# Kernel tuning notes

Measured on AMD Instinct MI355X. Metric: run time of the kernel, lower is better.

The kernel has to match this reference:

```python
import jax, jax.numpy as jnp
import numpy as np
import math

D_MODEL = 512
NUM_HEADS = 8
D_HEAD = D_MODEL // NUM_HEADS
B, S = 4, 2048
L = 2 * S - 1  # relative position range


def _rel_shift(pos_score):
    # pos_score: [B, H, S, L] -> [B, H, S, L//2+1] via pad/reshape/slice trick
    b, h, s, l = pos_score.shape
    padded = jnp.pad(pos_score, ((0, 0), (0, 0), (0, 0), (1, 0)))  # [B,H,S,L+1]
    padded = padded.reshape(b, h, l + 1, s)
    shifted = padded[:, :, 1:].reshape(b, h, s, l)
    return shifted[..., : l // 2 + 1]


def setup_inputs() -> dict:
    key = jax.random.key(0)
    ks = jax.random.split(key, 16)
    std = 1.0 / math.sqrt(D_MODEL)
    inp = {
        "query": jax.random.normal(ks[0], (B, S, D_MODEL), jnp.float32),
        "key": jax.random.normal(ks[1], (B, S, D_MODEL), jnp.float32),
        "value": jax.random.normal(ks[2], (B, S, D_MODEL), jnp.float32),
        "pos_embedding": jax.random.normal(ks[3], (B, L, D_MODEL), jnp.float32),
        "Wq": jax.random.normal(ks[4], (D_MODEL, D_MODEL), jnp.float32) * std,
        "bq": jnp.zeros((D_MODEL,), jnp.float32),
        "Wk": jax.random.normal(ks[5], (D_MODEL, D_MODEL), jnp.float32) * std,
        "bk": jnp.zeros((D_MODEL,), jnp.float32),
        "Wv": jax.random.normal(ks[6], (D_MODEL, D_MODEL), jnp.float32) * std,
        "bv": jnp.zeros((D_MODEL,), jnp.float32),
        "Wp": jax.random.normal(ks[7], (D_MODEL, D_MODEL), jnp.float32) * std,
        "u_bias": jax.random.normal(ks[8], (NUM_HEADS, D_HEAD), jnp.float32) * std,
        "v_bias": jax.random.normal(ks[9], (NUM_HEADS, D_HEAD), jnp.float32) * std,
        "Wo": jax.random.normal(ks[10], (D_MODEL, D_MODEL), jnp.float32) * std,
        "bo": jnp.zeros((D_MODEL,), jnp.float32),
    }
    return inp


def reference(query, key, value, pos_embedding, Wq, bq, Wk, bk, Wv, bv, Wp, u_bias, v_bias, Wo, bo):
    b, s, d = query.shape
    h, dh = u_bias.shape
    sqrt_dim = jnp.asarray(math.sqrt(d), query.dtype)

    q = (query @ Wq.T + bq).reshape(b, s, h, dh)
    k = (key @ Wk.T + bk).reshape(b, -1, h, dh)
    v = (value @ Wv.T + bv).reshape(b, -1, h, dh)
    p = (pos_embedding @ Wp.T).reshape(b, -1, h, dh)

    content_score = jnp.einsum("bshd,bthd->bhst", q + u_bias, k)
    pos_score = jnp.einsum("bshd,blhd->bhsl", q + v_bias, p)
    pos_score = _rel_shift(pos_score)  # [B,H,S,S]

    score = (content_score + pos_score) / sqrt_dim
    attn = jax.nn.softmax(score, axis=-1)
    context = jnp.einsum("bhst,bthd->bshd", attn, v).reshape(b, s, d)
    return context @ Wo.T + bo
```

## Files before the change

### kernel.cpp

```cpp
#include <hip/hip_runtime.h>


typedef __bf16 bf16;
typedef __bf16 bf16x4 __attribute__((ext_vector_type(4)));
typedef __bf16 bf16x8 __attribute__((ext_vector_type(8)));
typedef float  f32x4  __attribute__((ext_vector_type(4)));

#define MFMA(A,B,C) __builtin_amdgcn_mfma_f32_16x16x32_bf16((A),(B),(C),0,0,0)

constexpr float SCP = 1.44269504088896f / 22.6274169979695f;

__device__ __forceinline__ void gload16(const void* g, void* l) {
    __builtin_amdgcn_global_load_lds(
        (const __attribute__((address_space(1))) void*)g,
        (__attribute__((address_space(3))) void*)l, 16, 0, 0);
}

constexpr size_t WBYTES   = 512u*512u*2u;
constexpr size_t OFF_WQ   = 0;
constexpr size_t OFF_WK   = OFF_WQ + WBYTES;
constexpr size_t OFF_WV   = OFF_WK + WBYTES;
constexpr size_t OFF_WP   = OFF_WV + WBYTES;
constexpr size_t OFF_WO   = OFF_WP + WBYTES;
constexpr size_t QKV_BYTES = 4ull*8*2048*64*2;
constexpr size_t OFF_QU   = OFF_WO + WBYTES;
constexpr size_t OFF_QV   = OFF_QU + QKV_BYTES;
constexpr size_t OFF_KK   = OFF_QV + QKV_BYTES;
constexpr size_t OFF_VT   = OFF_KK + QKV_BYTES;
constexpr size_t OFF_PP   = OFF_VT + QKV_BYTES;
constexpr size_t PP_BYTES = 4ull*8*4096*64*2;
constexpr size_t OFF_CTX  = OFF_PP + PP_BYTES;

__global__ __launch_bounds__(256) void convert_weights(
    const float* __restrict__ w0, const float* __restrict__ w1,
    const float* __restrict__ w2, const float* __restrict__ w3,
    const float* __restrict__ w4, bf16* __restrict__ dst)
{
    int idx = blockIdx.x * 256 + threadIdx.x;
    const float* srcs[5] = {w0, w1, w2, w3, w4};
    int which = idx >> 15;
    int off   = (idx & 32767) * 8;
    const float* s = srcs[which] + off;
    float4 a = *(const float4*)s;
    float4 b = *(const float4*)(s + 4);
    bf16x8 o;
    o[0]=(bf16)a.x; o[1]=(bf16)a.y; o[2]=(bf16)a.z; o[3]=(bf16)a.w;
    o[4]=(bf16)b.x; o[5]=(bf16)b.y; o[6]=(bf16)b.z; o[7]=(bf16)b.w;
    *(bf16x8*)(dst + (size_t)which * (512*512) + off) = o;
}

__global__ __launch_bounds__(256) void gemm_proj(
    const float* __restrict__ Aq, const float* __restrict__ Ak,
    const float* __restrict__ Av, const float* __restrict__ Ap,
    const bf16* __restrict__ Wqb, const bf16* __restrict__ Wkb,
    const bf16* __restrict__ Wvb, const bf16* __restrict__ Wpb,
    const float* __restrict__ bq, const float* __restrict__ bk,
    const float* __restrict__ bv,
    const float* __restrict__ ub, const float* __restrict__ vb,
    bf16* __restrict__ qu, bf16* __restrict__ qv, bf16* __restrict__ kk,
    bf16* __restrict__ vt, bf16* __restrict__ pp)
{
    const int bid = blockIdx.x;
    const int mode = (bid < 768) ? (bid >> 8) : 3;
    const int idx  = (bid < 768) ? (bid & 255) : (bid - 768);
    const float* A  = (mode == 0) ? Aq  : (mode == 1) ? Ak  : (mode == 2) ? Av  : Ap;
    const bf16*  Bw = (mode == 0) ? Wqb : (mode == 1) ? Wkb : (mode == 2) ? Wvb : Wpb;

    __shared__ __align__(16) bf16 As[128 * 64];
    const int tid = threadIdx.x, lane = tid & 63, w = tid >> 6;
    const int r = lane & 15, g = lane >> 4;
    const int m0 = (idx >> 2) * 128, n0 = (idx & 3) * 128;
    const int wr = (w >> 1) * 64, wc = (w & 1) * 64;
    f32x4 acc[4][4] = {};

    for (int kt = 0; kt < 512; kt += 64) {
        __syncthreads();
        #pragma unroll
        for (int i = 0; i < 4; i++) {
            int gi = tid + 256 * i;
            int row = gi >> 3, c8 = gi & 7;
            int gm = m0 + row;
            float4 a0 = {0,0,0,0}, a1 = {0,0,0,0};
            if (mode != 3 || gm < 16380) {
                const float* ap = A + (size_t)gm * 512 + kt + c8 * 8;
                a0 = *(const float4*)ap;
                a1 = *(const float4*)(ap + 4);
            }
            bf16x8 v8;
            v8[0]=(bf16)a0.x; v8[1]=(bf16)a0.y; v8[2]=(bf16)a0.z; v8[3]=(bf16)a0.w;
            v8[4]=(bf16)a1.x; v8[5]=(bf16)a1.y; v8[6]=(bf16)a1.z; v8[7]=(bf16)a1.w;
            *(bf16x8*)((char*)As + row * 128 + ((c8 ^ (row & 7)) << 4)) = v8;
        }
        __syncthreads();
        #pragma unroll
        for (int ks = 0; ks < 2; ks++) {
            bf16x8 af[4], bfr[4];
            #pragma unroll
            for (int rt = 0; rt < 4; rt++) {
                int row = wr + rt * 16 + r;
                af[rt] = *(const bf16x8*)((const char*)As + row * 128 +
                                          (((ks * 4 + g) ^ (row & 7)) << 4));
            }
            #pragma unroll
            for (int ct = 0; ct < 4; ct++) {
                int n = n0 + wc + ct * 16 + r;
                bfr[ct] = *(const bf16x8*)(Bw + (size_t)n * 512 + kt + ks * 32 + g * 8);
            }
            #pragma unroll
            for (int rt = 0; rt < 4; rt++)
                #pragma unroll
                for (int ct = 0; ct < 4; ct++)
                    acc[rt][ct] = MFMA(af[rt], bfr[ct], acc[rt][ct]);
        }
    }

    #pragma unroll
    for (int rt = 0; rt < 4; rt++) {
        #pragma unroll
        for (int ct = 0; ct < 4; ct++) {
            int gn = n0 + wc + ct * 16 + r;
            int rb = m0 + wr + rt * 16 + g * 4;
            #pragma unroll
            for (int i = 0; i < 4; i++) {
                int gm = rb + i;
                float val = acc[rt][ct][i];
                if (mode == 0) {
                    int b = gm >> 11, s = gm & 2047, h = gn >> 6, dh = gn & 63;
                    size_t o = ((size_t)((b * 8 + h) * 2048 + s)) * 64 + dh;
                    float qb = val + bq[gn];
                    qu[o] = (bf16)((qb + ub[gn]) * SCP);
                    qv[o] = (bf16)((qb + vb[gn]) * SCP);
                } else if (mode == 1) {
                    int b = gm >> 11, s = gm & 2047, h = gn >> 6, dh = gn & 63;
                    kk[((size_t)((b * 8 + h) * 2048 + s)) * 64 +
                       (dh ^ ((s & 7) << 3))] = (bf16)(val + bk[gn]);
                } else if (mode == 2) {
                    int b = gm >> 11, s = gm & 2047, h = gn >> 6, dh = gn & 63;
                    int sc = s & 63, sb = s & ~63;
                    vt[((size_t)((b * 8 + h) * 64 + dh)) * 2048 + sb +
                       (sc ^ ((dh & 7) << 3))] = (bf16)(val + bv[gn]);
                } else {
                    if (gm < 16380) {
                        int b = gm / 4095, l = gm - b * 4095, h = gn >> 6, dh = gn & 63;
                        pp[((size_t)((b * 8 + h) * 4096 + l)) * 64 + dh] = (bf16)val;
                    }
                }
            }
        }
    }
}

__global__ __launch_bounds__(256) void gemm_out(
    const bf16* __restrict__ Ac, const bf16* __restrict__ Bw,
    const float* __restrict__ bias, float* __restrict__ of)
{
    __shared__ __align__(16) bf16 As[128 * 64];
    const int tid = threadIdx.x, lane = tid & 63, w = tid >> 6;
    const int r = lane & 15, g = lane >> 4;
    const int m0 = blockIdx.x * 128, n0 = blockIdx.y * 128;
    const int wr = (w >> 1) * 64, wc = (w & 1) * 64;
    f32x4 acc[4][4] = {};

    for (int kt = 0; kt < 512; kt += 64) {
        __syncthreads();
        #pragma unroll
        for (int i = 0; i < 4; i++) {
            int gi = tid + 256 * i;
            int row = gi >> 3, c8 = gi & 7;
            bf16x8 v8 = *(const bf16x8*)(Ac + (size_t)(m0 + row) * 512 + kt + c8 * 8);
            *(bf16x8*)((char*)As + row * 128 + ((c8 ^ (row & 7)) << 4)) = v8;
        }
        __syncthreads();
        #pragma unroll
        for (int ks = 0; ks < 2; ks++) {
            bf16x8 af[4], bfr[4];
            #pragma unroll
            for (int rt = 0; rt < 4; rt++) {
                int row = wr + rt * 16 + r;
                af[rt] = *(const bf16x8*)((const char*)As + row * 128 +
                                          (((ks * 4 + g) ^ (row & 7)) << 4));
            }
            #pragma unroll
            for (int ct = 0; ct < 4; ct++) {
                int n = n0 + wc + ct * 16 + r;
                bfr[ct] = *(const bf16x8*)(Bw + (size_t)n * 512 + kt + ks * 32 + g * 8);
            }
            #pragma unroll
            for (int rt = 0; rt < 4; rt++)
                #pragma unroll
                for (int ct = 0; ct < 4; ct++)
                    acc[rt][ct] = MFMA(af[rt], bfr[ct], acc[rt][ct]);
        }
    }
    #pragma unroll
    for (int rt = 0; rt < 4; rt++)
        #pragma unroll
        for (int ct = 0; ct < 4; ct++) {
            int gn = n0 + wc + ct * 16 + r;
            int rb = m0 + wr + rt * 16 + g * 4;
            #pragma unroll
            for (int i = 0; i < 4; i++)
                of[(size_t)(rb + i) * 512 + gn] = acc[rt][ct][i] + bias[gn];
        }
}

__global__ __launch_bounds__(512, 2) void attn_k(
    const bf16* __restrict__ qu, const bf16* __restrict__ qv,
    const bf16* __restrict__ kk, const bf16* __restrict__ vt,
    const bf16* __restrict__ pp, bf16* __restrict__ ctx)
{
    __shared__ __align__(16) bf16 kls[2][64 * 64];
    __shared__ __align__(16) bf16 vls[3][64 * 64];
    __shared__ __align__(16) bf16 ps2[256][100];
    __shared__ __align__(16) bf16 at_t[256 * 64];

    const int lane = threadIdx.x & 63, w = threadIdx.x >> 6;
    const int r = lane & 15, g = lane >> 4;
    const int sw = (r & 7) << 4;
    const int bid = blockIdx.x;
    const int lbid = (bid & 7) * 32 + (bid >> 3);
    const int bh = lbid >> 3;
    const int sigma = lbid & 7;
    const int s0 = sigma << 8;
    const int qb = w << 5;

    const bf16* quB = qu + (size_t)bh * 2048 * 64;
    const bf16* qvB = qv + (size_t)bh * 2048 * 64;
    const bf16* kkB = kk + (size_t)bh * 2048 * 64;
    const bf16* vtB = vt + (size_t)bh * 64 * 2048;
    const bf16* ppB = pp + (size_t)bh * 4096 * 64;

    bf16x8 qaf[2][2], qvf[2][2];
    #pragma unroll
    for (int qs = 0; qs < 2; qs++) {
        const int srow = s0 + qb + qs * 16 + r;
        qaf[qs][0] = *(const bf16x8*)(quB + (size_t)srow * 64 + g * 8);
        qaf[qs][1] = *(const bf16x8*)(quB + (size_t)srow * 64 + 32 + g * 8);
        qvf[qs][0] = *(const bf16x8*)(qvB + (size_t)srow * 64 + g * 8);
        qvf[qs][1] = *(const bf16x8*)(qvB + (size_t)srow * 64 + 32 + g * 8);
    }
    __builtin_amdgcn_sched_barrier(0);

    const int lq = lane >> 3, lc = (lane & 7) << 4;

    bf16x8 pfP[12];
    {
        const int tp = ((sigma * 4) & 31) << 6;
        gload16((const char*)kkB + ((size_t)(tp + w * 8 + lq) << 7) + lc,
                (char*)kls[0] + w * 1024);
        gload16((const char*)vtB + ((size_t)(w * 8 + lq) << 12) + tp * 2 + lc,
                (char*)vls[0] + w * 1024);
        __builtin_amdgcn_sched_barrier(0);
        const int lbw = tp - s0 - qb + 2016;
        #pragma unroll
        for (int j = 0; j < 6; j++) {
            const bf16* pr = ppB + (size_t)(lbw + j * 16 + r) * 64 + g * 8;
            pfP[2*j]   = *(const bf16x8*)pr;
            pfP[2*j+1] = *(const bf16x8*)(pr + 32);
        }
        asm volatile("s_waitcnt vmcnt(0)" ::: "memory");
        __builtin_amdgcn_s_barrier();
        __builtin_amdgcn_sched_barrier(0);
    }

    f32x4 oacc[2][4] = {};
    float sums[2] = {0.f, 0.f};
    int iv_prev = 2, iv_cur = 0, iv_next = 1;

    #pragma unroll 2
    for (int n = 0; n < 32; ++n) {
        const int cur = n & 1;
        if (n > 0) {
            __builtin_amdgcn_s_barrier();
            __builtin_amdgcn_sched_barrier(0);
        }

        {
            const int tn = ((sigma * 4 + n + 1) & 31) << 6;
            gload16((const char*)kkB + ((size_t)(tn + w * 8 + lq) << 7) + lc,
                    (char*)kls[cur ^ 1] + w * 1024);
            gload16((const char*)vtB + ((size_t)(w * 8 + lq) << 12) + tn * 2 + lc,
                    (char*)vls[iv_next] + w * 1024);
        }
        __builtin_amdgcn_sched_barrier(0);

        if (n > 0) {
            const char* vbase = (const char*)vls[iv_prev];
            #pragma unroll
            for (int ks = 0; ks < 2; ks++) {
                bf16x8 af[2];
                #pragma unroll
                for (int qs = 0; qs < 2; qs++)
                    af[qs] = *(const bf16x8*)((const char*)at_t +
                               (qb + qs * 16 + r) * 128 + ((ks * 64 + g * 16) ^ sw));
                #pragma unroll
                for (int nt = 0; nt < 4; nt++) {
                    bf16x8 vf = *(const bf16x8*)(vbase + (nt * 16 + r) * 128 +
                                                 ((ks * 64 + g * 16) ^ sw));
                    oacc[0][nt] = MFMA(af[0], vf, oacc[0][nt]);
                    oacc[1][nt] = MFMA(af[1], vf, oacc[1][nt]);
                }
            }
        }

        #pragma unroll
        for (int j = 0; j < 6; j++) {
            #pragma unroll
            for (int qs = 0; qs < 2; qs++) {
                f32x4 ps = {};
                ps = MFMA(pfP[2*j],   qvf[qs][0], ps);
                ps = MFMA(pfP[2*j+1], qvf[qs][1], ps);
                bf16x4 pb;
                pb[0]=(bf16)ps[0]; pb[1]=(bf16)ps[1]; pb[2]=(bf16)ps[2]; pb[3]=(bf16)ps[3];
                *(bf16x4*)(&ps2[qb + qs * 16 + r][j * 16 + g * 4]) = pb;
            }
        }

        {
            const int tn  = ((sigma * 4 + n + 1) & 31) << 6;
            const int lbw = tn - s0 - qb + 2016;
            #pragma unroll
            for (int j = 0; j < 6; j++) {
                const bf16* pr = ppB + (size_t)(lbw + j * 16 + r) * 64 + g * 8;
                pfP[2*j]   = *(const bf16x8*)pr;
                pfP[2*j+1] = *(const bf16x8*)(pr + 32);
            }
        }

        f32x4 cc[2][4];
        #pragma unroll
        for (int c = 0; c < 4; c++) {
            const char* kb = (const char*)kls[cur] + (c * 16 + r) * 128;
            bf16x8 k0 = *(const bf16x8*)(kb + (( 0 + g * 16) ^ sw));
            bf16x8 k1 = *(const bf16x8*)(kb + ((64 + g * 16) ^ sw));
            #pragma unroll
            for (int qs = 0; qs < 2; qs++) {
                f32x4 a = {};
                a = MFMA(k0, qaf[qs][0], a);
                a = MFMA(k1, qaf[qs][1], a);
                cc[qs][c] = a;
            }
        }

        #pragma unroll
        for (int qs = 0; qs < 2; qs++) {
            const bf16* prow = &ps2[qb + qs * 16 + r][0];
            #pragma unroll
            for (int c = 0; c < 4; c++) {
                const int base = c * 16 + g * 4 + 31 - qs * 16 - r;
                float p0 = prow[base], p1 = prow[base+1], p2 = prow[base+2], p3 = prow[base+3];
                float e0 = exp2f(cc[qs][c][0] + p0);
                float e1 = exp2f(cc[qs][c][1] + p1);
                float e2 = exp2f(cc[qs][c][2] + p2);
                float e3 = exp2f(cc[qs][c][3] + p3);
                sums[qs] += (e0 + e1) + (e2 + e3);
                bf16x4 pk;
                pk[0]=(bf16)e0; pk[1]=(bf16)e1; pk[2]=(bf16)e2; pk[3]=(bf16)e3;
                *(bf16x4*)((char*)at_t + (qb + qs * 16 + r) * 128 +
                           ((c * 32 + g * 8) ^ sw)) = pk;
            }
        }

        #pragma unroll
        for (int j = 0; j < 12; j++)
            asm volatile("" : "+v"(pfP[j]));

        const int t_ = iv_prev; iv_prev = iv_cur; iv_cur = iv_next; iv_next = t_;
    }

    asm volatile("s_waitcnt vmcnt(0)" ::: "memory");

    {
        const char* vbase = (const char*)vls[iv_prev];
        #pragma unroll
        for (int ks = 0; ks < 2; ks++) {
            bf16x8 af[2];
            #pragma unroll
            for (int qs = 0; qs < 2; qs++)
                af[qs] = *(const bf16x8*)((const char*)at_t +
                           (qb + qs * 16 + r) * 128 + ((ks * 64 + g * 16) ^ sw));
            #pragma unroll
            for (int nt = 0; nt < 4; nt++) {
                bf16x8 vf = *(const bf16x8*)(vbase + (nt * 16 + r) * 128 +
                                             ((ks * 64 + g * 16) ^ sw));
                oacc[0][nt] = MFMA(af[0], vf, oacc[0][nt]);
                oacc[1][nt] = MFMA(af[1], vf, oacc[1][nt]);
            }
        }
    }

    const int b = bh >> 3, h = bh & 7;
    #pragma unroll
    for (int qs = 0; qs < 2; qs++) {
        float sm = sums[qs];
        sm += __shfl_xor(sm, 16);
        sm += __shfl_xor(sm, 32);
        const float inv = 1.f / sm;
        #pragma unroll
        for (int nt = 0; nt < 4; nt++) {
            #pragma unroll
            for (int i = 0; i < 4; i++) {
                const float si = __shfl(inv, g * 4 + i);
                const int s = s0 + qb + qs * 16 + g * 4 + i;
                const int col = h * 64 + nt * 16 + r;
                ctx[((size_t)(b * 2048 + s)) * 512 + col] = (bf16)(oacc[qs][nt][i] * si);
            }
        }
    }
}

extern "C" void kernel_launch(void* const* d_in, const int* in_sizes, int n_in,
                              void* d_out, int out_size, void* d_ws, size_t ws_size,
                              hipStream_t stream)
{
    (void)in_sizes; (void)n_in; (void)out_size; (void)ws_size;
    const float* query = (const float*)d_in[0];
    const float* key_  = (const float*)d_in[1];
    const float* value = (const float*)d_in[2];
    const float* pos   = (const float*)d_in[3];
    const float* Wq = (const float*)d_in[4];  const float* bq = (const float*)d_in[5];
    const float* Wk = (const float*)d_in[6];  const float* bk = (const float*)d_in[7];
    const float* Wv = (const float*)d_in[8];  const float* bv = (const float*)d_in[9];
    const float* Wp = (const float*)d_in[10];
    const float* ub = (const float*)d_in[11]; const float* vb = (const float*)d_in[12];
    const float* Wo = (const float*)d_in[13]; const float* bo = (const float*)d_in[14];

    char* ws = (char*)d_ws;
    bf16* Wqb = (bf16*)(ws + OFF_WQ);
    bf16* Wkb = (bf16*)(ws + OFF_WK);
    bf16* Wvb = (bf16*)(ws + OFF_WV);
    bf16* Wpb = (bf16*)(ws + OFF_WP);
    bf16* Wob = (bf16*)(ws + OFF_WO);
    bf16* quP = (bf16*)(ws + OFF_QU);
    bf16* qvP = (bf16*)(ws + OFF_QV);
    bf16* kkP = (bf16*)(ws + OFF_KK);
    bf16* vtP = (bf16*)(ws + OFF_VT);
    bf16* ppP = (bf16*)(ws + OFF_PP);
    bf16* ctxP = (bf16*)(ws + OFF_CTX);

    convert_weights<<<640, 256, 0, stream>>>(Wq, Wk, Wv, Wp, Wo, (bf16*)(ws + OFF_WQ));

    gemm_proj<<<dim3(1280), 256, 0, stream>>>(
        query, key_, value, pos, Wqb, Wkb, Wvb, Wpb,
        bq, bk, bv, ub, vb, quP, qvP, kkP, vtP, ppP);

    attn_k<<<dim3(256), 512, 0, stream>>>(quP, qvP, kkP, vtP, ppP, ctxP);

    gemm_out<<<dim3(64, 4), 256, 0, stream>>>(ctxP, Wob, bo, (float*)d_out);
}
```

Baseline: 255.1 us.

## Skip unused positional MFMA tiles, hoist LDS addressing, use raw v_exp and packed loads

```diff
diff --git a/kernel.cpp b/kernel.cpp
--- a/kernel.cpp
+++ b/kernel.cpp
@@ -14,6 +14,12 @@
     __builtin_amdgcn_global_load_lds(
         (const __attribute__((address_space(1))) void*)g,
         (__attribute__((address_space(3))) void*)l, 16, 0, 0);
+}
+
+__device__ __forceinline__ float fexp2(float x) {
+    float y;
+    asm("v_exp_f32 %0, %1" : "=v"(y) : "v"(x));
+    return y;
 }
 
 constexpr size_t WBYTES   = 512u*512u*2u;
@@ -243,6 +249,22 @@
 
     const int lq = lane >> 3, lc = (lane & 7) << 4;
 
+    const int ko0 = (g * 16) ^ sw, ko1 = (64 + g * 16) ^ sw;
+    const char* kb0 = (const char*)kls + r * 128 + ko0;
+    const char* kb1 = (const char*)kls + r * 128 + ko1;
+    const char* vb0 = (const char*)vls + r * 128 + ko0;
+    const char* vb1 = (const char*)vls + r * 128 + ko1;
+    char* atw = (char*)at_t + (qb + r) * 128;
+    const int as_[4] = { (0 + g*8) ^ sw, (32 + g*8) ^ sw,
+                         (64 + g*8) ^ sw, (96 + g*8) ^ sw };
+    bf16* psw0 = &ps2[qb + r][g * 4];
+    bf16* psw1 = &ps2[qb + 16 + r][g * 4];
+    const int base00 = g * 4 + 31 - r;
+    const int base01 = g * 4 + 15 - r;
+    const uint32_t* psd0 = (const uint32_t*)&ps2[qb + r][0] + (base00 >> 1);
+    const uint32_t* psd1 = (const uint32_t*)&ps2[qb + 16 + r][0] + (base01 >> 1);
+    const int sh0 = (base00 & 1) << 4, sh1 = (base01 & 1) << 4;
+
     bf16x8 pfP[12];
     {
         const int tp = ((sigma * 4) & 31) << 6;
@@ -285,18 +307,15 @@
         __builtin_amdgcn_sched_barrier(0);
 
         if (n > 0) {
-            const char* vbase = (const char*)vls[iv_prev];
+            const int vo = iv_prev * 8192;
             #pragma unroll
             for (int ks = 0; ks < 2; ks++) {
                 bf16x8 af[2];
-                #pragma unroll
-                for (int qs = 0; qs < 2; qs++)
-                    af[qs] = *(const bf16x8*)((const char*)at_t +
-                               (qb + qs * 16 + r) * 128 + ((ks * 64 + g * 16) ^ sw));
+                af[0] = *(const bf16x8*)(atw + (ks ? ko1 : ko0));
+                af[1] = *(const bf16x8*)(atw + 2048 + (ks ? ko1 : ko0));
                 #pragma unroll
                 for (int nt = 0; nt < 4; nt++) {
-                    bf16x8 vf = *(const bf16x8*)(vbase + (nt * 16 + r) * 128 +
-                                                 ((ks * 64 + g * 16) ^ sw));
+                    bf16x8 vf = *(const bf16x8*)((ks ? vb1 : vb0) + vo + nt * 2048);
                     oacc[0][nt] = MFMA(af[0], vf, oacc[0][nt]);
                     oacc[1][nt] = MFMA(af[1], vf, oacc[1][nt]);
                 }
@@ -305,14 +324,21 @@
 
         #pragma unroll
         for (int j = 0; j < 6; j++) {
-            #pragma unroll
-            for (int qs = 0; qs < 2; qs++) {
+            if (j < 5) {
                 f32x4 ps = {};
-                ps = MFMA(pfP[2*j],   qvf[qs][0], ps);
-                ps = MFMA(pfP[2*j+1], qvf[qs][1], ps);
+                ps = MFMA(pfP[2*j],   qvf[1][0], ps);
+                ps = MFMA(pfP[2*j+1], qvf[1][1], ps);
                 bf16x4 pb;
                 pb[0]=(bf16)ps[0]; pb[1]=(bf16)ps[1]; pb[2]=(bf16)ps[2]; pb[3]=(bf16)ps[3];
-                *(bf16x4*)(&ps2[qb + qs * 16 + r][j * 16 + g * 4]) = pb;
+                *(bf16x4*)(psw1 + j * 16) = pb;
+            }
+            if (j > 0) {
+                f32x4 ps = {};
+                ps = MFMA(pfP[2*j],   qvf[0][0], ps);
+                ps = MFMA(pfP[2*j+1], qvf[0][1], ps);
+                bf16x4 pb;
+                pb[0]=(bf16)ps[0]; pb[1]=(bf16)ps[1]; pb[2]=(bf16)ps[2]; pb[3]=(bf16)ps[3];
+                *(bf16x4*)(psw0 + j * 16) = pb;
             }
         }
 
@@ -330,9 +356,8 @@
         f32x4 cc[2][4];
         #pragma unroll
         for (int c = 0; c < 4; c++) {
-            const char* kb = (const char*)kls[cur] + (c * 16 + r) * 128;
-            bf16x8 k0 = *(const bf16x8*)(kb + (( 0 + g * 16) ^ sw));
-            bf16x8 k1 = *(const bf16x8*)(kb + ((64 + g * 16) ^ sw));
+            bf16x8 k0 = *(const bf16x8*)(kb0 + cur * 8192 + c * 2048);
+            bf16x8 k1 = *(const bf16x8*)(kb1 + cur * 8192 + c * 2048);
             #pragma unroll
             for (int qs = 0; qs < 2; qs++) {
                 f32x4 a = {};
@@ -344,20 +369,25 @@
 
         #pragma unroll
         for (int qs = 0; qs < 2; qs++) {
-            const bf16* prow = &ps2[qb + qs * 16 + r][0];
+            const uint32_t* P = qs ? psd1 : psd0;
+            const int sh = qs ? sh1 : sh0;
             #pragma unroll
             for (int c = 0; c < 4; c++) {
-                const int base = c * 16 + g * 4 + 31 - qs * 16 - r;
-                float p0 = prow[base], p1 = prow[base+1], p2 = prow[base+2], p3 = prow[base+3];
-                float e0 = exp2f(cc[qs][c][0] + p0);
-                float e1 = exp2f(cc[qs][c][1] + p1);
-                float e2 = exp2f(cc[qs][c][2] + p2);
-                float e3 = exp2f(cc[qs][c][3] + p3);
+                uint32_t d0 = P[8*c], d1 = P[8*c + 1], d2 = P[8*c + 2];
+                uint32_t e01 = __builtin_amdgcn_alignbit(d1, d0, sh);
+                uint32_t e23 = __builtin_amdgcn_alignbit(d2, d1, sh);
+                float p0 = __builtin_bit_cast(float, e01 << 16);
+                float p1 = __builtin_bit_cast(float, e01 & 0xffff0000u);
+                float p2 = __builtin_bit_cast(float, e23 << 16);
+                float p3 = __builtin_bit_cast(float, e23 & 0xffff0000u);
+                float e0 = fexp2(cc[qs][c][0] + p0);
+                float e1 = fexp2(cc[qs][c][1] + p1);
+                float e2 = fexp2(cc[qs][c][2] + p2);
+                float e3 = fexp2(cc[qs][c][3] + p3);
                 sums[qs] += (e0 + e1) + (e2 + e3);
                 bf16x4 pk;
                 pk[0]=(bf16)e0; pk[1]=(bf16)e1; pk[2]=(bf16)e2; pk[3]=(bf16)e3;
-                *(bf16x4*)((char*)at_t + (qb + qs * 16 + r) * 128 +
-                           ((c * 32 + g * 8) ^ sw)) = pk;
+                *(bf16x4*)(atw + qs * 2048 + as_[c]) = pk;
             }
         }
 
@@ -371,18 +401,15 @@
     asm volatile("s_waitcnt vmcnt(0)" ::: "memory");
 
     {
-        const char* vbase = (const char*)vls[iv_prev];
+        const int vo = iv_prev * 8192;
         #pragma unroll
         for (int ks = 0; ks < 2; ks++) {
             bf16x8 af[2];
-            #pragma unroll
-            for (int qs = 0; qs < 2; qs++)
-                af[qs] = *(const bf16x8*)((const char*)at_t +
-                           (qb + qs * 16 + r) * 128 + ((ks * 64 + g * 16) ^ sw));
+            af[0] = *(const bf16x8*)(atw + (ks ? ko1 : ko0));
+            af[1] = *(const bf16x8*)(atw + 2048 + (ks ? ko1 : ko0));
             #pragma unroll
             for (int nt = 0; nt < 4; nt++) {
-                bf16x8 vf = *(const bf16x8*)(vbase + (nt * 16 + r) * 128 +
-                                             ((ks * 64 + g * 16) ^ sw));
+                bf16x8 vf = *(const bf16x8*)((ks ? vb1 : vb0) + vo + nt * 2048);
                 oacc[0][nt] = MFMA(af[0], vf, oacc[0][nt]);
                 oacc[1][nt] = MFMA(af[1], vf, oacc[1][nt]);
             }
```

Result: faster. 249.0 us (-2.4%).
